# Performance work log

Hardware: AMD Instinct MI355X
Metric: run time of the kernel (lower is better)

Reference implementation:

```python
import jax, jax.numpy as jnp
import numpy as np

B, SC, ST = 16, 512, 512
DP, DC = 256, 128
D = DP + 2 * DC          # 512 = d_model
H, L, DFF = 8, 2, 2048
NCAT, NCONT = 1000, 2048


def sin_embed(vals, d, scale=1000.0):
    # vectorized sinusoidal_time_embedding: even dims -> sin(angle), odd dims -> cos(angle)
    i = jnp.arange(d, dtype=jnp.float32)
    ang = vals.astype(jnp.float32)[..., None] / jnp.power(scale, i / d)
    return jnp.where(i % 2 == 0, jnp.sin(ang), jnp.cos(ang))


def layer_norm(x, g, b, eps=1e-5):
    m = jnp.mean(x, -1, keepdims=True)
    v = jnp.mean(jnp.square(x - m), -1, keepdims=True)
    return (x - m) / jnp.sqrt(v + eps) * g + b


def setup_inputs() -> dict:
    key = jax.random.key(0)
    ks = jax.random.split(key, 16)
    s = 0.02
    def n(k, shape, scale=s):
        return jax.random.normal(k, shape, dtype=jnp.float32) * scale
    return {
        "context_cat": jax.random.randint(ks[0], (B, SC), 0, NCAT),
        "context_time": jax.random.uniform(ks[1], (B, SC), dtype=jnp.float32) * 100.0,
        "context_f0": jax.random.uniform(ks[2], (B, SC), dtype=jnp.float32) * 500.0,
        "target_cat": jax.random.randint(ks[3], (B, ST), 0, NCAT),
        "target_time": jax.random.uniform(ks[4], (B, ST), dtype=jnp.float32) * 100.0,
        "target_f0": jax.random.uniform(ks[5], (B, ST), dtype=jnp.float32) * 500.0,
        "cat_table": n(ks[6], (NCAT, DP), 1.0),
        "cont_table": sin_embed(jnp.arange(NCONT, dtype=jnp.float32), DC),  # frozen sin table
        "pad_emb": n(ks[7], (D,), 1.0),
        "Wq": n(ks[8], (L, D, D)), "bq": jnp.zeros((L, D)),
        "Wk": n(ks[9], (L, D, D)), "bk": jnp.zeros((L, D)),
        "Wv": n(ks[10], (L, D, D)), "bv": jnp.zeros((L, D)),
        "Wo": n(ks[11], (L, D, D)), "bo": jnp.zeros((L, D)),
        "ln1g": jnp.ones((L, D)), "ln1b": jnp.zeros((L, D)),
        "ln2g": jnp.ones((L, D)), "ln2b": jnp.zeros((L, D)),
        "W1": n(ks[12], (L, D, DFF)), "b1": jnp.zeros((L, DFF)),
        "W2": n(ks[13], (L, DFF, D)), "b2": jnp.zeros((L, D)),
    }


def reference(context_cat, context_time, context_f0, target_cat, target_time, target_f0,
              cat_table, cont_table, pad_emb,
              Wq, bq, Wk, bk, Wv, bv, Wo, bo,
              ln1g, ln1b, ln2g, ln2b, W1, b1, W2, b2):
    def embed(cat, tm, f0):
        pad = cat < 0
        e = jnp.concatenate(
            [cat_table[jnp.maximum(cat, 0)], sin_embed(tm, DC), sin_embed(f0, DC)], axis=-1)
        return jnp.where(pad[..., None], pad_emb, e), pad

    ce, cp = embed(context_cat, context_time, context_f0)
    te, tp = embed(target_cat, target_time, target_f0)
    x = jnp.concatenate([ce, te], axis=1)                       # [B, SC+ST, D]
    bias = jnp.where(jnp.concatenate([cp, tp], 1), -1e9, 0.0)[:, None, None, :]
    hd = D // H
    inv_sqrt = 1.0 / np.sqrt(hd).astype(np.float32)

    def step(h, p):
        wq, bq_, wk, bk_, wv, bv_, wo, bo_, g1, c1, g2, c2, w1, d1, w2, d2 = p
        Bn, S, _ = h.shape
        q = (h @ wq + bq_).reshape(Bn, S, H, hd)
        k = (h @ wk + bk_).reshape(Bn, S, H, hd)
        v = (h @ wv + bv_).reshape(Bn, S, H, hd)
        scores = jnp.einsum('bqhd,bkhd->bhqk', q, k) * inv_sqrt + bias
        attn = jax.nn.softmax(scores, axis=-1)
        o = jnp.einsum('bhqk,bkhd->bqhd', attn, v).reshape(Bn, S, D)
        h = layer_norm(h + o @ wo + bo_, g1, c1)                # post-norm (torch default)
        f = jax.nn.relu(h @ w1 + d1) @ w2 + d2
        return layer_norm(h + f, g2, c2), None

    x, _ = jax.lax.scan(step, x, (Wq, bq, Wk, bk, Wv, bv, Wo, bo,
                                  ln1g, ln1b, ln2g, ln2b, W1, b1, W2, b2))
    out = x[:, SC:, :]
    pred_cat = out[..., :DP] @ cat_table.T
    pred_time = out[..., DP:DP + DC] @ cont_table.T
    pred_f0 = out[..., DP + DC:] @ cont_table.T
    return pred_cat, pred_time, pred_f0
```

## Files before the change

### kernel.cpp

```cpp
#include <hip/hip_runtime.h>


typedef _Float16 half8 __attribute__((ext_vector_type(8)));
typedef _Float16 half4 __attribute__((ext_vector_type(4)));
typedef float f32x4 __attribute__((ext_vector_type(4)));
typedef unsigned int uint2v __attribute__((ext_vector_type(2)));
typedef unsigned int uint4v __attribute__((ext_vector_type(4)));

__device__ __forceinline__ void gl2lds16(const _Float16* g, _Float16* l) {
    __builtin_amdgcn_global_load_lds(
        (const __attribute__((address_space(1))) void*)g,
        (__attribute__((address_space(3))) void*)l, 16, 0, 0);
}

__global__ void cast_f32_f16_k(const float* __restrict__ in, _Float16* __restrict__ out,
                               long nsrc, long ntot) {
    long i = (long)blockIdx.x * blockDim.x + threadIdx.x;
    long stride = (long)gridDim.x * blockDim.x;
    for (; i < ntot; i += stride) out[i] = i < nsrc ? (_Float16)in[i] : (_Float16)0.f;
}

__global__ void tcast_k(const float* __restrict__ in, _Float16* __restrict__ out,
                        int R, int C, long zs, int rowoff) {
    __shared__ float tile[32][33];
    long z = blockIdx.z;
    const float* src = in + z * (long)R * C;
    _Float16* dst = out + z * zs + (long)rowoff * R;
    int c0 = blockIdx.x * 32, r0 = blockIdx.y * 32;
    for (int i = threadIdx.y; i < 32; i += 8)
        tile[i][threadIdx.x] = src[(long)(r0 + i) * C + c0 + threadIdx.x];
    __syncthreads();
    for (int i = threadIdx.y; i < 32; i += 8)
        dst[(long)(c0 + i) * R + r0 + threadIdx.x] = (_Float16)tile[threadIdx.x][i];
}

__global__ void bcat_k(const float* __restrict__ bq, const float* __restrict__ bk,
                       const float* __restrict__ bv, float* __restrict__ out, int L) {
    int i = blockIdx.x * 256 + threadIdx.x;
    if (i >= L * 1536) return;
    int l = i / 1536, j = i - l * 1536;
    float v = j < 512 ? bq[l * 512 + j] : (j < 1024 ? bk[l * 512 + j - 512] : bv[l * 512 + j - 1024]);
    out[i] = v;
}

__global__ void vtrans_k(const _Float16* __restrict__ qkv, _Float16* __restrict__ vT) {
    __shared__ _Float16 tile[32][33];
    int bh = blockIdx.z; int b = bh >> 3, h = bh & 7;
    int s0 = blockIdx.x * 32, d0 = blockIdx.y * 32;
    const _Float16* src = qkv + ((long)b * 1024) * 1536 + 1024 + h * 64;
    _Float16* dst = vT + (long)bh * 64 * 1024;
    for (int i = threadIdx.y; i < 32; i += 8)
        tile[i][threadIdx.x] = src[(long)(s0 + i) * 1536 + d0 + threadIdx.x];
    __syncthreads();
    for (int i = threadIdx.y; i < 32; i += 8)
        dst[(long)(d0 + i) * 1024 + s0 + threadIdx.x] = tile[threadIdx.x][i];
}

__global__ __launch_bounds__(128) void embed_k(
    const int* __restrict__ ccat, const float* __restrict__ ctime, const float* __restrict__ cf0,
    const int* __restrict__ tcat, const float* __restrict__ ttime, const float* __restrict__ tf0,
    const float* __restrict__ cat_table, const float* __restrict__ pad_emb,
    _Float16* __restrict__ xb, float* __restrict__ biasKey) {
    int t = blockIdx.x;
    int b = t >> 10, s = t & 1023;
    int j = b * 512 + (s & 511);
    int cat; float tm, f0;
    if (s < 512) { cat = ccat[j]; tm = ctime[j]; f0 = cf0[j]; }
    else         { cat = tcat[j]; tm = ttime[j]; f0 = tf0[j]; }
    bool pad = cat < 0;
    if (threadIdx.x == 0) biasKey[t] = pad ? -1e9f : 0.f;
    int c = cat < 0 ? 0 : cat;
    half4 h4;
    #pragma unroll
    for (int u = 0; u < 4; u++) {
        int d = threadIdx.x * 4 + u;
        float val;
        if (pad) val = pad_emb[d];
        else if (d < 256) val = cat_table[(long)c * 256 + d];
        else {
            float base = (d < 384) ? tm : f0;
            int i = (d < 384) ? (d - 256) : (d - 384);
            float ang = base / powf(1000.f, (float)i * (1.f / 128.f));
            val = (i & 1) ? cosf(ang) : sinf(ang);
        }
        h4[u] = (_Float16)val;
    }
    *(half4*)&xb[(long)t * 512 + threadIdx.x * 4] = h4;
}

__global__ __launch_bounds__(256) void layernorm_k(
    const _Float16* __restrict__ in, _Float16* __restrict__ out,
    const float* __restrict__ g, const float* __restrict__ beta) {
    long row = blockIdx.x;
    int tid = threadIdx.x;
    const unsigned* rw = (const unsigned*)(in + row * 512);
    unsigned wo = rw[tid];
    float v0 = (float)(_Float16)__builtin_bit_cast(_Float16, (unsigned short)(wo & 0xffff));
    float v1 = (float)(_Float16)__builtin_bit_cast(_Float16, (unsigned short)(wo >> 16));
    float s = v0 + v1, q = v0 * v0 + v1 * v1;
    #pragma unroll
    for (int o = 32; o; o >>= 1) { s += __shfl_down(s, o); q += __shfl_down(q, o); }
    __shared__ float rs[4], rq[4];
    if ((tid & 63) == 0) { rs[tid >> 6] = s; rq[tid >> 6] = q; }
    __syncthreads();
    s = rs[0] + rs[1] + rs[2] + rs[3];
    q = rq[0] + rq[1] + rq[2] + rq[3];
    float mean = s * (1.f / 512.f);
    float var = q * (1.f / 512.f) - mean * mean;
    float rstd = rsqrtf(var + 1e-5f);
    float y0 = (v0 - mean) * rstd * g[tid * 2] + beta[tid * 2];
    float y1 = (v1 - mean) * rstd * g[tid * 2 + 1] + beta[tid * 2 + 1];
    unsigned short u0 = __builtin_bit_cast(unsigned short, (_Float16)y0);
    unsigned short u1 = __builtin_bit_cast(unsigned short, (_Float16)y1);
    ((unsigned*)(out + row * 512))[tid] = (unsigned)u0 | ((unsigned)u1 << 16);
}

__global__ __launch_bounds__(512, 4) void flash_k(
    const _Float16* __restrict__ QKV, const _Float16* __restrict__ VT,
    const float* __restrict__ biasKey, _Float16* __restrict__ O) {
    const int S = 1024, D = 512, LDQ = 1536, NT = 16;
    int bh = blockIdx.x; int b = bh >> 3, h = bh & 7;
    int qt = blockIdx.y;
    int tid = threadIdx.x, w = tid >> 6, lane = tid & 63;
    int g = lane >> 4, q15 = lane & 15;

    __shared__ __align__(16) _Float16 Ks[2][64 * 64];
    __shared__ __align__(16) _Float16 VTs[2][64 * 64];
    __shared__ __align__(16) float biasLds[1024];

    {
        const float* bsrc = biasKey + (long)b * S;
        biasLds[tid]       = bsrc[tid] * 1.442695041f;
        biasLds[tid + 512] = bsrc[tid + 512] * 1.442695041f;
    }

    int qrow = qt * 128 + w * 16 + q15;
    const _Float16* qp = QKV + ((long)(b * S + qrow)) * LDQ + h * 64 + g * 8;
    half8 qf[2];
    qf[0] = *(const half8*)(qp);
    qf[1] = *(const half8*)(qp + 32);
    const _Float16 qsc = (_Float16)0.1803368801f;
    #pragma unroll
    for (int kk = 0; kk < 2; kk++)
        #pragma unroll
        for (int i = 0; i < 8; i++) qf[kk][i] *= qsc;

    const _Float16* kbase = QKV + 512 + ((long)b * S) * LDQ + h * 64;
    const _Float16* vbase = VT + (long)bh * 64 * S;

    auto stageK = [&](int buf, int kt) {
        int row = tid >> 3, p = tid & 7;
        int s = p ^ (row & 7);
        gl2lds16(kbase + (long)(kt * 64 + row) * LDQ + s * 8, &Ks[buf][tid * 8]);
    };
    auto stageV = [&](int buf, int kt) {
        int row = tid >> 3, p = tid & 7;
        int s = p ^ (row & 7);
        gl2lds16(vbase + (long)row * S + kt * 64 + s * 8, &VTs[buf][tid * 8]);
    };

    f32x4 acc_o[4];
    #pragma unroll
    for (int i = 0; i < 4; i++)
        #pragma unroll
        for (int r = 0; r < 4; r++) acc_o[i][r] = 0.f;
    float m_run = -1e30f, l_run = 0.f;
    bool gOdd = (g & 1) != 0;

    auto QK = [&](int kt, f32x4 (&s)[4]) {
        #pragma unroll
        for (int mf = 0; mf < 4; mf++)
            s[mf] = *(const f32x4*)&biasLds[kt * 64 + mf * 16 + g * 4];
        int buf = kt & 1;
        __builtin_amdgcn_s_setprio(1);
        #pragma unroll
        for (int kk = 0; kk < 2; kk++)
            #pragma unroll
            for (int mf = 0; mf < 4; mf++) {
                int row = mf * 16 + q15;
                half8 kf = *(const half8*)&Ks[buf][row * 64 + (((kk * 4 + g) ^ (row & 7)) * 8)];
                s[mf] = __builtin_amdgcn_mfma_f32_16x16x32_f16(kf, qf[kk], s[mf], 0, 0, 0);
            }
        __builtin_amdgcn_s_setprio(0);
    };

    auto SMPV = [&](int kt, f32x4 (&s)[4]) {
        float t0 = fmaxf(fmaxf(s[0][0], s[0][1]), fmaxf(s[0][2], s[0][3]));
        float t1 = fmaxf(fmaxf(s[1][0], s[1][1]), fmaxf(s[1][2], s[1][3]));
        float t2 = fmaxf(fmaxf(s[2][0], s[2][1]), fmaxf(s[2][2], s[2][3]));
        float t3 = fmaxf(fmaxf(s[3][0], s[3][1]), fmaxf(s[3][2], s[3][3]));
        float mt = fmaxf(fmaxf(t0, t1), fmaxf(t2, t3));
        mt = fmaxf(mt, __shfl_xor(mt, 16));
        mt = fmaxf(mt, __shfl_xor(mt, 32));

        float rsum = 0.f;
        if (__all(mt - m_run <= 8.f)) {
            #pragma unroll
            for (int mf = 0; mf < 4; mf++)
                #pragma unroll
                for (int r = 0; r < 4; r++) {
                    float p = exp2f(s[mf][r] - m_run);
                    s[mf][r] = p; rsum += p;
                }
        } else {
            float m_new = fmaxf(m_run, mt);
            float scale = exp2f(m_run - m_new);
            #pragma unroll
            for (int mf = 0; mf < 4; mf++)
                #pragma unroll
                for (int r = 0; r < 4; r++) {
                    float p = exp2f(s[mf][r] - m_new);
                    s[mf][r] = p; rsum += p;
                }
            float sc[4];
            #pragma unroll
            for (int r = 0; r < 4; r++) sc[r] = __shfl(scale, g * 4 + r);
            #pragma unroll
            for (int nf = 0; nf < 4; nf++)
                #pragma unroll
                for (int r = 0; r < 4; r++) acc_o[nf][r] *= sc[r];
            l_run *= scale;
            m_run = m_new;
        }
        rsum += __shfl_xor(rsum, 16);
        rsum += __shfl_xor(rsum, 32);
        l_run += rsum;

        unsigned pk[4][2];
        #pragma unroll
        for (int mf = 0; mf < 4; mf++) {
            auto h0 = __builtin_amdgcn_cvt_pkrtz(s[mf][0], s[mf][1]);
            auto h1 = __builtin_amdgcn_cvt_pkrtz(s[mf][2], s[mf][3]);
            pk[mf][0] = __builtin_bit_cast(unsigned, h0);
            pk[mf][1] = __builtin_bit_cast(unsigned, h1);
        }

        int buf = kt & 1;
        #pragma unroll
        for (int kk = 0; kk < 2; kk++) {
            unsigned wA[2], wB[2];
            #pragma unroll
            for (int wi = 0; wi < 2; wi++) {
                uint2v r2 = __builtin_amdgcn_permlane32_swap(
                    pk[2 * kk][wi], pk[2 * kk + 1][wi], false, false);
                unsigned na = r2[0];
                unsigned nb = r2[1];
                unsigned sa = (unsigned)__builtin_amdgcn_ds_swizzle((int)na, 0x401F);
                unsigned sb = (unsigned)__builtin_amdgcn_ds_swizzle((int)nb, 0x401F);
                wA[wi] = gOdd ? sb : na;
                wB[wi] = gOdd ? nb : sa;
            }
            uint4v paw;
            paw[0] = wA[0]; paw[1] = wA[1]; paw[2] = wB[0]; paw[3] = wB[1];
            half8 pa = __builtin_bit_cast(half8, paw);
            __builtin_amdgcn_s_setprio(1);
            #pragma unroll
            for (int nf = 0; nf < 4; nf++) {
                int row = nf * 16 + q15;
                half8 vf = *(const half8*)&VTs[buf][row * 64 + (((kk * 4 + g) ^ (row & 7)) * 8)];
                acc_o[nf] = __builtin_amdgcn_mfma_f32_16x16x32_f16(pa, vf, acc_o[nf], 0, 0, 0);
            }
            __builtin_amdgcn_s_setprio(0);
        }
    };

    f32x4 sA[4], sB[4];
    stageK(0, 0); stageV(0, 0); stageK(1, 1);
    __syncthreads();
    QK(0, sA);

    for (int t = 0; t < NT; t += 2) {
        __syncthreads();
        if (t + 2 < NT) stageK(t & 1, t + 2);
        if (t + 1 < NT) stageV((t + 1) & 1, t + 1);
        if (t + 1 < NT) QK(t + 1, sB);
        SMPV(t, sA);
        __syncthreads();
        if (t + 3 < NT) stageK((t + 1) & 1, t + 3);
        if (t + 2 < NT) stageV(t & 1, t + 2);
        if (t + 2 < NT) QK(t + 2, sA);
        SMPV(t + 1, sB);
    }

    float linv = 1.f / l_run;
    float lv[4];
    #pragma unroll
    for (int r = 0; r < 4; r++) lv[r] = __shfl(linv, g * 4 + r);
    _Float16* obase = O + ((long)(b * S + qt * 128 + w * 16)) * D + h * 64;
    #pragma unroll
    for (int nf = 0; nf < 4; nf++)
        #pragma unroll
        for (int r = 0; r < 4; r++) {
            int row = g * 4 + r;
            obase[(long)row * D + nf * 16 + q15] = (_Float16)(acc_o[nf][r] * lv[r]);
        }
}

template<int MODE>
__global__ __launch_bounds__(256) void gemm_nt(
    const _Float16* __restrict__ A, long lda, long sA1, long sA2,
    const _Float16* __restrict__ Bm, long ldb, long sB1, long sB2,
    float* Cf, _Float16* Cb, long ldc, long sC1, long sC2,
    const float* __restrict__ bias, long sb1, long sb2,
    const _Float16* resid,
    int M, int N, int K, int Z2, float alpha, int relu) {
    constexpr int BK = MODE ? 64 : 32;
    constexpr int SLOTS = BK / 8;
    constexpr int LPS = (128 * BK / 8) / 256;

    int z = blockIdx.z;
    int z1 = z / Z2, z2 = z - z1 * Z2;
    A  += z1 * sA1 + z2 * sA2;
    Bm += z1 * sB1 + z2 * sB2;
    long coff = z1 * sC1 + z2 * sC2;
    if (bias) bias += z1 * sb1 + z2 * sb2;

    int gx = gridDim.x;
    int nwg = gx * gridDim.y;
    int bid = blockIdx.y * gx + blockIdx.x;
    int q = nwg >> 3, r = nwg & 7;
    int xcd = bid & 7, ii = bid >> 3;
    int swz = (xcd < r ? xcd * (q + 1) : r * (q + 1) + (xcd - r) * q) + ii;
    int m0 = (swz / gx) * 128;
    int n0 = (swz % gx) * 128;

    __shared__ __align__(16) _Float16 As[2][128 * BK];
    __shared__ __align__(16) _Float16 Bs[2][128 * BK];

    int tid = threadIdx.x;
    int lane = tid & 63;
    int w = tid >> 6;
    int wr = (w >> 1) << 6;
    int wc = (w & 1) << 6;

    f32x4 acc[4][4];
    #pragma unroll
    for (int i = 0; i < 4; i++)
        #pragma unroll
        for (int jj = 0; jj < 4; jj++) { acc[i][jj][0] = 0.f; acc[i][jj][1] = 0.f; acc[i][jj][2] = 0.f; acc[i][jj][3] = 0.f; }

    int fr = lane & 15;
    int g = lane >> 4;

    auto stage = [&](int buf, int kt) {
        #pragma unroll
        for (int i = 0; i < LPS; i++) {
            int idx = tid + i * 256;
            int row = idx / SLOTS, s = idx % SLOTS;
            int sg = s ^ (row & (SLOTS - 1));
            gl2lds16(A + (long)(m0 + row) * lda + kt * BK + sg * 8, &As[buf][idx * 8]);
            gl2lds16(Bm + (long)(n0 + row) * ldb + kt * BK + sg * 8, &Bs[buf][idx * 8]);
        }
    };

    auto compute = [&](int cur) {
        #pragma unroll
        for (int kk = 0; kk < BK / 32; kk++) {
            half8 af[4], bfv[4];
            #pragma unroll
            for (int m = 0; m < 4; m++) {
                int row = wr + m * 16 + fr;
                af[m] = *(const half8*)&As[cur][row * BK + (((kk * 4 + g) ^ (row & (SLOTS - 1))) * 8)];
            }
            #pragma unroll
            for (int n = 0; n < 4; n++) {
                int row = wc + n * 16 + fr;
                bfv[n] = *(const half8*)&Bs[cur][row * BK + (((kk * 4 + g) ^ (row & (SLOTS - 1))) * 8)];
            }
            #pragma unroll
            for (int m = 0; m < 4; m++)
                #pragma unroll
                for (int n = 0; n < 4; n++)
                    acc[m][n] = __builtin_amdgcn_mfma_f32_16x16x32_f16(af[m], bfv[n], acc[m][n], 0, 0, 0);
        }
    };

    int nk = K / BK;
    stage(0, 0);
    for (int t = 0; t < nk; ++t) {
        __builtin_amdgcn_s_barrier();
        if (t + 1 < nk) {
            stage((t + 1) & 1, t + 1);
            if constexpr (MODE == 0)
                asm volatile("s_waitcnt vmcnt(4)" ::: "memory");
            else
                asm volatile("s_waitcnt vmcnt(8)" ::: "memory");
        } else {
            asm volatile("s_waitcnt vmcnt(0)" ::: "memory");
        }
        __builtin_amdgcn_s_barrier();
        __builtin_amdgcn_sched_barrier(0);
        compute(t & 1);
    }

    int fq = lane >> 4;
    #pragma unroll
    for (int m = 0; m < 4; m++) {
        #pragma unroll
        for (int jj = 0; jj < 4; jj++) {
            long row = m0 + wr + m * 16 + fq * 4 + jj;
            #pragma unroll
            for (int n = 0; n < 4; n++) {
                int col = n0 + wc + n * 16 + fr;
                if (col < N) {
                    float v = acc[m][n][jj] * alpha;
                    if (bias) v += bias[col];
                    long o = coff + row * ldc + col;
                    if (resid) v += (float)resid[o];
                    if (relu) v = fmaxf(v, 0.f);
                    if (Cf) Cf[o] = v;
                    if (Cb) Cb[o] = (_Float16)v;
                }
            }
        }
    }
}

extern "C" void kernel_launch(void* const* d_in, const int* in_sizes, int n_in,
                              void* d_out, int out_size, void* d_ws, size_t ws_size,
                              hipStream_t stream) {
    const int Bn = 16, S = 1024, D = 512, H = 8, L = 2, DFF = 2048, NCAT = 1000, NCONT = 2048;
    const long M = (long)Bn * S;

    const int*   ccat      = (const int*)d_in[0];
    const float* ctime     = (const float*)d_in[1];
    const float* cf0       = (const float*)d_in[2];
    const int*   tcat      = (const int*)d_in[3];
    const float* ttime     = (const float*)d_in[4];
    const float* tf0       = (const float*)d_in[5];
    const float* cat_table = (const float*)d_in[6];
    const float* cont_tab  = (const float*)d_in[7];
    const float* pad_emb   = (const float*)d_in[8];
    const float* Wq = (const float*)d_in[9];
    const float* bq = (const float*)d_in[10];
    const float* Wk = (const float*)d_in[11];
    const float* bk = (const float*)d_in[12];
    const float* Wv = (const float*)d_in[13];
    const float* bv = (const float*)d_in[14];
    const float* Wo = (const float*)d_in[15];
    const float* bo = (const float*)d_in[16];
    const float* ln1g = (const float*)d_in[17];
    const float* ln1b = (const float*)d_in[18];
    const float* ln2g = (const float*)d_in[19];
    const float* ln2b = (const float*)d_in[20];
    const float* W1 = (const float*)d_in[21];
    const float* b1 = (const float*)d_in[22];
    const float* W2 = (const float*)d_in[23];
    const float* b2 = (const float*)d_in[24];

    char* wsb = (char*)d_ws;
    size_t off = 0;
    auto alloc = [&](size_t bytes) -> void* {
        off = (off + 255) & ~(size_t)255;
        void* p = wsb + off; off += bytes; return p;
    };

    _Float16*  xb      = (_Float16*)alloc(M * D * 2);
    _Float16*  tb      = (_Float16*)alloc(M * D * 2);
    _Float16*  hb      = (_Float16*)alloc(M * D * 2);
    _Float16*  qkv     = (_Float16*)alloc(M * 3 * D * 2);
    _Float16*  vT      = (_Float16*)alloc(M * D * 2);
    _Float16*  ob      = (_Float16*)alloc(M * D * 2);
    float*     biasKey = (float*)alloc(M * 4);
    _Float16*  WqkvT = (_Float16*)alloc((size_t)L * 3 * D * D * 2);
    float*     bqkv  = (float*)alloc((size_t)L * 3 * D * 4);
    _Float16*  WoT  = (_Float16*)alloc((size_t)L * D * D * 2);
    _Float16*  W1T  = (_Float16*)alloc((size_t)L * D * DFF * 2);
    _Float16*  W2T  = (_Float16*)alloc((size_t)L * DFF * D * 2);
    _Float16*  catT = (_Float16*)alloc((size_t)1024 * 256 * 2);
    _Float16*  conT = (_Float16*)alloc((size_t)NCONT * 128 * 2);

    size_t need_ffh = (size_t)M * DFF * 2;
    _Float16* ffh;
    size_t offAl = (off + 255) & ~(size_t)255;
    if (offAl + need_ffh <= ws_size) ffh = (_Float16*)alloc(need_ffh);
    else ffh = (_Float16*)d_out;

    auto gemm = [&](const _Float16* A, long lda, long sA1, long sA2,
                    const _Float16* Bm, long ldb, long sB1, long sB2,
                    float* Cf, _Float16* Cb, long ldc, long sC1, long sC2,
                    const float* bias, long sb1, long sb2,
                    const _Float16* resid, int Mm, int Nn, int Kk,
                    int Z1, int Z2, float alpha, int relu, int deep) {
        dim3 gdim((Nn + 127) / 128, (Mm + 127) / 128, Z1 * Z2);
        if (deep)
            gemm_nt<1><<<gdim, 256, 0, stream>>>(A, lda, sA1, sA2, Bm, ldb, sB1, sB2,
                                                 Cf, Cb, ldc, sC1, sC2, bias, sb1, sb2,
                                                 resid, Mm, Nn, Kk, Z2, alpha, relu);
        else
            gemm_nt<0><<<gdim, 256, 0, stream>>>(A, lda, sA1, sA2, Bm, ldb, sB1, sB2,
                                                 Cf, Cb, ldc, sC1, sC2, bias, sb1, sb2,
                                                 resid, Mm, Nn, Kk, Z2, alpha, relu);
    };

    dim3 tb8(32, 8);
    tcast_k<<<dim3(D / 32, D / 32, L), tb8, 0, stream>>>(Wq, WqkvT, D, D, (long)3 * D * D, 0);
    tcast_k<<<dim3(D / 32, D / 32, L), tb8, 0, stream>>>(Wk, WqkvT, D, D, (long)3 * D * D, D);
    tcast_k<<<dim3(D / 32, D / 32, L), tb8, 0, stream>>>(Wv, WqkvT, D, D, (long)3 * D * D, 2 * D);
    bcat_k<<<dim3((L * 1536 + 255) / 256), 256, 0, stream>>>(bq, bk, bv, bqkv, L);
    tcast_k<<<dim3(D / 32, D / 32, L), tb8, 0, stream>>>(Wo, WoT, D, D, (long)D * D, 0);
    tcast_k<<<dim3(DFF / 32, D / 32, L), tb8, 0, stream>>>(W1, W1T, D, DFF, (long)D * DFF, 0);
    tcast_k<<<dim3(D / 32, DFF / 32, L), tb8, 0, stream>>>(W2, W2T, DFF, D, (long)DFF * D, 0);
    cast_f32_f16_k<<<dim3(512), 256, 0, stream>>>(cat_table, catT, (long)NCAT * 256, (long)1024 * 256);
    cast_f32_f16_k<<<dim3(512), 256, 0, stream>>>(cont_tab, conT, (long)NCONT * 128, (long)NCONT * 128);

    embed_k<<<dim3((unsigned)M), 128, 0, stream>>>(ccat, ctime, cf0, tcat, ttime, tf0,
                                                   cat_table, pad_emb, xb, biasKey);

    for (int l = 0; l < L; l++) {
        gemm(xb, D, 0, 0, WqkvT + (size_t)l * 3 * D * D, D, 0, 0, nullptr, qkv, 3 * D, 0, 0,
             bqkv + (size_t)l * 3 * D, 0, 0, nullptr, (int)M, 3 * D, D, 1, 1, 1.f, 0, 0);
        vtrans_k<<<dim3(32, 2, Bn * H), tb8, 0, stream>>>(qkv, vT);

        flash_k<<<dim3(Bn * H, S / 128), 512, 0, stream>>>(qkv, vT, biasKey, ob);

        gemm(ob, D, 0, 0, WoT + (size_t)l * D * D, D, 0, 0, nullptr, tb, D, 0, 0,
             bo + l * D, 0, 0, xb, (int)M, D, D, 1, 1, 1.f, 0, 1);
        layernorm_k<<<dim3((unsigned)M), 256, 0, stream>>>(tb, hb, ln1g + l * D, ln1b + l * D);

        gemm(hb, D, 0, 0, W1T + (size_t)l * D * DFF, D, 0, 0, nullptr, ffh, DFF, 0, 0,
             b1 + l * DFF, 0, 0, nullptr, (int)M, DFF, D, 1, 1, 1.f, 1, 0);
        gemm(ffh, DFF, 0, 0, W2T + (size_t)l * DFF * D, DFF, 0, 0, nullptr, tb, D, 0, 0,
             b2 + l * D, 0, 0, hb, (int)M, D, DFF, 1, 1, 1.f, 0, 1);
        layernorm_k<<<dim3((unsigned)M), 256, 0, stream>>>(tb, xb, ln2g + l * D, ln2b + l * D);
    }

    float* out_cat  = (float*)d_out;
    float* out_time = out_cat + (size_t)Bn * 512 * NCAT;
    float* out_f0   = out_time + (size_t)Bn * 512 * NCONT;
    gemm(xb + (size_t)512 * D, D, (long)S * D, 0,
         catT, 256, 0, 0,
         out_cat, nullptr, NCAT, (long)512 * NCAT, 0,
         nullptr, 0, 0, nullptr, 512, NCAT, 256, Bn, 1, 1.f, 0, 0);
    gemm(xb + (size_t)512 * D + 256, D, (long)S * D, 128,
         conT, 128, 0, 0,
         out_time, nullptr, NCONT, (long)512 * NCONT, (long)Bn * 512 * NCONT,
         nullptr, 0, 0, nullptr, 512, NCONT, 128, Bn, 2, 1.f, 0, 0);
}
```

Measured before the change: 812.5 us.

## Use 128-key tiles in flash attention and one wave per row in layernorm

The flash attention kernel now processes keys in tiles of 128 instead of 64. This halves the loop trips and barriers, and it swaps the two-tile software pipeline (QK of the next tile overlapped with softmax/PV of the current one) for a simpler single-tile loop with double-buffered staging. The layernorm kernel now handles four rows per block, one wavefront per row, with 16-byte vector loads and stores and shuffle-only reductions, which drops the shared-memory step and the barrier. The larger attention tiles double LDS use and score registers, which may lower occupancy and lose the QK/softmax overlap.

```diff
diff --git a/kernel.cpp b/kernel.cpp
--- a/kernel.cpp
+++ b/kernel.cpp
@@ -91,41 +91,42 @@
 __global__ __launch_bounds__(256) void layernorm_k(
     const _Float16* __restrict__ in, _Float16* __restrict__ out,
     const float* __restrict__ g, const float* __restrict__ beta) {
-    long row = blockIdx.x;
-    int tid = threadIdx.x;
-    const unsigned* rw = (const unsigned*)(in + row * 512);
-    unsigned wo = rw[tid];
-    float v0 = (float)(_Float16)__builtin_bit_cast(_Float16, (unsigned short)(wo & 0xffff));
-    float v1 = (float)(_Float16)__builtin_bit_cast(_Float16, (unsigned short)(wo >> 16));
-    float s = v0 + v1, q = v0 * v0 + v1 * v1;
-    #pragma unroll
-    for (int o = 32; o; o >>= 1) { s += __shfl_down(s, o); q += __shfl_down(q, o); }
-    __shared__ float rs[4], rq[4];
-    if ((tid & 63) == 0) { rs[tid >> 6] = s; rq[tid >> 6] = q; }
-    __syncthreads();
-    s = rs[0] + rs[1] + rs[2] + rs[3];
-    q = rq[0] + rq[1] + rq[2] + rq[3];
+    int wv = threadIdx.x >> 6, lane = threadIdx.x & 63;
+    long row = (long)blockIdx.x * 4 + wv;
+    half8 hv = *(const half8*)(in + row * 512 + lane * 8);
+    float v[8];
+    float s = 0.f, q = 0.f;
+    #pragma unroll
+    for (int u = 0; u < 8; u++) {
+        v[u] = (float)hv[u];
+        s += v[u];
+        q += v[u] * v[u];
+    }
+    #pragma unroll
+    for (int o = 32; o; o >>= 1) { s += __shfl_xor(s, o); q += __shfl_xor(q, o); }
     float mean = s * (1.f / 512.f);
     float var = q * (1.f / 512.f) - mean * mean;
     float rstd = rsqrtf(var + 1e-5f);
-    float y0 = (v0 - mean) * rstd * g[tid * 2] + beta[tid * 2];
-    float y1 = (v1 - mean) * rstd * g[tid * 2 + 1] + beta[tid * 2 + 1];
-    unsigned short u0 = __builtin_bit_cast(unsigned short, (_Float16)y0);
-    unsigned short u1 = __builtin_bit_cast(unsigned short, (_Float16)y1);
-    ((unsigned*)(out + row * 512))[tid] = (unsigned)u0 | ((unsigned)u1 << 16);
+    half8 hy;
+    #pragma unroll
+    for (int u = 0; u < 8; u++) {
+        float y = (v[u] - mean) * rstd * g[lane * 8 + u] + beta[lane * 8 + u];
+        hy[u] = (_Float16)y;
+    }
+    *(half8*)(out + row * 512 + lane * 8) = hy;
 }
 
 __global__ __launch_bounds__(512, 4) void flash_k(
     const _Float16* __restrict__ QKV, const _Float16* __restrict__ VT,
     const float* __restrict__ biasKey, _Float16* __restrict__ O) {
-    const int S = 1024, D = 512, LDQ = 1536, NT = 16;
+    const int S = 1024, D = 512, LDQ = 1536, NT = 8;
     int bh = blockIdx.x; int b = bh >> 3, h = bh & 7;
     int qt = blockIdx.y;
     int tid = threadIdx.x, w = tid >> 6, lane = tid & 63;
     int g = lane >> 4, q15 = lane & 15;
 
-    __shared__ __align__(16) _Float16 Ks[2][64 * 64];
-    __shared__ __align__(16) _Float16 VTs[2][64 * 64];
+    __shared__ __align__(16) _Float16 Ks[2][128 * 64];
+    __shared__ __align__(16) _Float16 VTs[2][64 * 128];
     __shared__ __align__(16) float biasLds[1024];
 
     {
@@ -149,14 +150,22 @@
     const _Float16* vbase = VT + (long)bh * 64 * S;
 
     auto stageK = [&](int buf, int kt) {
-        int row = tid >> 3, p = tid & 7;
-        int s = p ^ (row & 7);
-        gl2lds16(kbase + (long)(kt * 64 + row) * LDQ + s * 8, &Ks[buf][tid * 8]);
+        #pragma unroll
+        for (int i = 0; i < 2; i++) {
+            int idx = tid + i * 512;
+            int row = idx >> 3, p = idx & 7;
+            int s = p ^ (row & 7);
+            gl2lds16(kbase + (long)(kt * 128 + row) * LDQ + s * 8, &Ks[buf][idx * 8]);
+        }
     };
     auto stageV = [&](int buf, int kt) {
-        int row = tid >> 3, p = tid & 7;
-        int s = p ^ (row & 7);
-        gl2lds16(vbase + (long)row * S + kt * 64 + s * 8, &VTs[buf][tid * 8]);
+        #pragma unroll
+        for (int i = 0; i < 2; i++) {
+            int idx = tid + i * 512;
+            int row = idx >> 4, p = idx & 15;
+            int s = p ^ (row & 15);
+            gl2lds16(vbase + (long)row * S + kt * 128 + s * 8, &VTs[buf][idx * 8]);
+        }
     };
 
     f32x4 acc_o[4];
@@ -167,36 +176,42 @@
     float m_run = -1e30f, l_run = 0.f;
     bool gOdd = (g & 1) != 0;
 
-    auto QK = [&](int kt, f32x4 (&s)[4]) {
-        #pragma unroll
-        for (int mf = 0; mf < 4; mf++)
-            s[mf] = *(const f32x4*)&biasLds[kt * 64 + mf * 16 + g * 4];
-        int buf = kt & 1;
+    f32x4 s[8];
+    stageK(0, 0); stageV(0, 0);
+    __syncthreads();
+
+    for (int t = 0; t < NT; t++) {
+        if (t) __syncthreads();
+        int buf = t & 1;
+        if (t + 1 < NT) { stageK(buf ^ 1, t + 1); stageV(buf ^ 1, t + 1); }
+
+        #pragma unroll
+        for (int mf = 0; mf < 8; mf++)
+            s[mf] = *(const f32x4*)&biasLds[t * 128 + mf * 16 + g * 4];
         __builtin_amdgcn_s_setprio(1);
         #pragma unroll
         for (int kk = 0; kk < 2; kk++)
             #pragma unroll
-            for (int mf = 0; mf < 4; mf++) {
+            for (int mf = 0; mf < 8; mf++) {
                 int row = mf * 16 + q15;
                 half8 kf = *(const half8*)&Ks[buf][row * 64 + (((kk * 4 + g) ^ (row & 7)) * 8)];
                 s[mf] = __builtin_amdgcn_mfma_f32_16x16x32_f16(kf, qf[kk], s[mf], 0, 0, 0);
             }
         __builtin_amdgcn_s_setprio(0);
-    };
-
-    auto SMPV = [&](int kt, f32x4 (&s)[4]) {
-        float t0 = fmaxf(fmaxf(s[0][0], s[0][1]), fmaxf(s[0][2], s[0][3]));
-        float t1 = fmaxf(fmaxf(s[1][0], s[1][1]), fmaxf(s[1][2], s[1][3]));
-        float t2 = fmaxf(fmaxf(s[2][0], s[2][1]), fmaxf(s[2][2], s[2][3]));
-        float t3 = fmaxf(fmaxf(s[3][0], s[3][1]), fmaxf(s[3][2], s[3][3]));
-        float mt = fmaxf(fmaxf(t0, t1), fmaxf(t2, t3));
+
+        float mt = -1e30f;
+        #pragma unroll
+        for (int mf = 0; mf < 8; mf++) {
+            float a = fmaxf(fmaxf(s[mf][0], s[mf][1]), fmaxf(s[mf][2], s[mf][3]));
+            mt = fmaxf(mt, a);
+        }
         mt = fmaxf(mt, __shfl_xor(mt, 16));
         mt = fmaxf(mt, __shfl_xor(mt, 32));
 
         float rsum = 0.f;
         if (__all(mt - m_run <= 8.f)) {
             #pragma unroll
-            for (int mf = 0; mf < 4; mf++)
+            for (int mf = 0; mf < 8; mf++)
                 #pragma unroll
                 for (int r = 0; r < 4; r++) {
                     float p = exp2f(s[mf][r] - m_run);
@@ -206,7 +221,7 @@
             float m_new = fmaxf(m_run, mt);
             float scale = exp2f(m_run - m_new);
             #pragma unroll
-            for (int mf = 0; mf < 4; mf++)
+            for (int mf = 0; mf < 8; mf++)
                 #pragma unroll
                 for (int r = 0; r < 4; r++) {
                     float p = exp2f(s[mf][r] - m_new);
@@ -226,18 +241,17 @@
         rsum += __shfl_xor(rsum, 32);
         l_run += rsum;
 
-        unsigned pk[4][2];
-        #pragma unroll
-        for (int mf = 0; mf < 4; mf++) {
+        unsigned pk[8][2];
+        #pragma unroll
+        for (int mf = 0; mf < 8; mf++) {
             auto h0 = __builtin_amdgcn_cvt_pkrtz(s[mf][0], s[mf][1]);
             auto h1 = __builtin_amdgcn_cvt_pkrtz(s[mf][2], s[mf][3]);
             pk[mf][0] = __builtin_bit_cast(unsigned, h0);
             pk[mf][1] = __builtin_bit_cast(unsigned, h1);
         }
 
-        int buf = kt & 1;
-        #pragma unroll
-        for (int kk = 0; kk < 2; kk++) {
+        #pragma unroll
+        for (int kk = 0; kk < 4; kk++) {
             unsigned wA[2], wB[2];
             #pragma unroll
             for (int wi = 0; wi < 2; wi++) {
@@ -257,29 +271,11 @@
             #pragma unroll
             for (int nf = 0; nf < 4; nf++) {
                 int row = nf * 16 + q15;
-                half8 vf = *(const half8*)&VTs[buf][row * 64 + (((kk * 4 + g) ^ (row & 7)) * 8)];
+                half8 vf = *(const half8*)&VTs[buf][row * 128 + (((kk * 4 + g) ^ (row & 15)) * 8)];
                 acc_o[nf] = __builtin_amdgcn_mfma_f32_16x16x32_f16(pa, vf, acc_o[nf], 0, 0, 0);
             }
             __builtin_amdgcn_s_setprio(0);
         }
-    };
-
-    f32x4 sA[4], sB[4];
-    stageK(0, 0); stageV(0, 0); stageK(1, 1);
-    __syncthreads();
-    QK(0, sA);
-
-    for (int t = 0; t < NT; t += 2) {
-        __syncthreads();
-        if (t + 2 < NT) stageK(t & 1, t + 2);
-        if (t + 1 < NT) stageV((t + 1) & 1, t + 1);
-        if (t + 1 < NT) QK(t + 1, sB);
-        SMPV(t, sA);
-        __syncthreads();
-        if (t + 3 < NT) stageK((t + 1) & 1, t + 3);
-        if (t + 2 < NT) stageV(t & 1, t + 2);
-        if (t + 2 < NT) QK(t + 2, sA);
-        SMPV(t + 1, sB);
     }
 
     float linv = 1.f / l_run;
@@ -516,13 +512,13 @@
 
         gemm(ob, D, 0, 0, WoT + (size_t)l * D * D, D, 0, 0, nullptr, tb, D, 0, 0,
              bo + l * D, 0, 0, xb, (int)M, D, D, 1, 1, 1.f, 0, 1);
-        layernorm_k<<<dim3((unsigned)M), 256, 0, stream>>>(tb, hb, ln1g + l * D, ln1b + l * D);
+        layernorm_k<<<dim3((unsigned)(M / 4)), 256, 0, stream>>>(tb, hb, ln1g + l * D, ln1b + l * D);
 
         gemm(hb, D, 0, 0, W1T + (size_t)l * D * DFF, D, 0, 0, nullptr, ffh, DFF, 0, 0,
              b1 + l * DFF, 0, 0, nullptr, (int)M, DFF, D, 1, 1, 1.f, 1, 0);
         gemm(ffh, DFF, 0, 0, W2T + (size_t)l * DFF * D, DFF, 0, 0, nullptr, tb, D, 0, 0,
              b2 + l * D, 0, 0, hb, (int)M, D, DFF, 1, 1, 1.f, 0, 1);
-        layernorm_k<<<dim3((unsigned)M), 256, 0, stream>>>(tb, xb, ln2g + l * D, ln2b + l * D);
+        layernorm_k<<<dim3((unsigned)(M / 4)), 256, 0, stream>>>(tb, xb, ln2g + l * D, ln2b + l * D);
     }
 
     float* out_cat  = (float*)d_out;
```

New measurement: 800.5 us. About the same (-1.5%).
